# Kernel tuning notes

Measured on AMD Instinct MI355X. Metric: run time of the kernel, lower is better.

Reference implementation:

```python
import jax, jax.numpy as jnp
import numpy as np

S = 20  # number of standard amino acids; hardcoded in the original layer


def expm_fixed(A, squarings=6, terms=14):
    """Scaling-and-squaring matrix exponential with fixed squaring count.
    A: (..., n, n). tau*Q entries are small (tau ~ softplus(-3)), so a fixed
    2^-6 scaling + Taylor-14 matches tf.linalg.expm to fp32 tolerance."""
    A = A / (2.0 ** squarings)
    I = jnp.broadcast_to(jnp.eye(A.shape[-1], dtype=A.dtype), A.shape)
    out = I
    term = I
    for i in range(1, terms + 1):
        term = jnp.matmul(term, A) / i
        out = out + term
    for _ in range(squarings):
        out = jnp.matmul(out, out)
    return out


def make_rate_matrix(R, p, eps=1e-16):
    """R: (N, s, s) symmetric exchangeabilities, zero diag. p: (N, s) equilibrium."""
    Q = R * p[:, None, :]                       # Q[i,j] = R[i,j] * p[j]
    diag = jnp.sum(Q, axis=-1, keepdims=True)   # (N, s, 1)
    eye = jnp.eye(Q.shape[-1], dtype=Q.dtype)
    Q = Q - diag * eye
    mue = jnp.sum(p[:, :, None] * diag, axis=-2, keepdims=True)  # (N,1,1)
    return Q / jnp.maximum(mue, eps)


def setup_inputs() -> dict:
    key = jax.random.key(0)
    ks = jax.random.split(key, 6)
    m, b, L, k, nr = 2, 256, 1024, 4, 100
    inputs = jax.random.uniform(ks[0], (m, b, L, S), dtype=jnp.float32)
    rate_indices = jax.random.randint(ks[1], (m, b), 0, nr, dtype=jnp.int64)
    # rate_init = constant(-3.0); small jitter so gradients are non-degenerate
    tau_kernel = -3.0 + 0.1 * jax.random.normal(ks[2], (m, nr), dtype=jnp.float32)
    exchangeability_kernel = 0.1 * jax.random.normal(ks[3], (m, k, S, S), dtype=jnp.float32)
    equilibrium_kernel = 0.1 * jax.random.normal(ks[4], (m, k, S), dtype=jnp.float32)
    per_matrix_rates_kernel = 0.1 * jax.random.normal(ks[5], (m, k), dtype=jnp.float32)
    return {
        "inputs": inputs,
        "tau_kernel": tau_kernel,
        "exchangeability_kernel": exchangeability_kernel,
        "equilibrium_kernel": equilibrium_kernel,
        "per_matrix_rates_kernel": per_matrix_rates_kernel,
        "rate_indices": rate_indices,
    }


def reference(inputs, tau_kernel, exchangeability_kernel, equilibrium_kernel,
              per_matrix_rates_kernel, rate_indices):
    m, b, L, s = inputs.shape
    k = exchangeability_kernel.shape[1]
    # make_tau(subset): gather per-sequence times then softplus
    tau = jax.nn.softplus(jnp.take_along_axis(tau_kernel, rate_indices, axis=1))  # (m,b)
    # per-matrix rates
    pmr = jax.nn.softplus(per_matrix_rates_kernel)  # (m,k)
    mut_rates = tau[:, :, None] * pmr[:, None, :]   # (m,b,k)
    # make_R: symmetrize, softplus, zero diagonal
    K = exchangeability_kernel
    R = jax.nn.softplus(0.5 * (K + jnp.swapaxes(K, -1, -2)))
    R = R * (1.0 - jnp.eye(s, dtype=R.dtype))       # (m,k,s,s)
    # make_p
    p = jax.nn.softmax(equilibrium_kernel, axis=-1)  # (m,k,s)
    # normalized rate matrices
    Q = make_rate_matrix(R.reshape(-1, s, s), p.reshape(-1, s)).reshape(m, k, s, s)
    # tau * Q, batched over sequences: (m,b,k,s,s)
    tauQ = mut_rates[..., None, None] * Q[:, None]
    P = expm_fixed(tauQ.reshape(-1, s, s)).reshape(m, b, k, s, s)
    # vector-format inputs path (non-transposed): mbLz,mbkzs->mbLks
    anc = jnp.einsum('mblz,mbkzs->mblks', inputs, P)
    # documented output: (num_model, b, L, num_matrices*s)
    return anc.reshape(m, b, L, k * s)
```

## Files before the change

kernel.cpp:

```cpp
#include <hip/hip_runtime.h>
#include <math.h>

#define M_  2
#define B_  256
#define L_  1024
#define K_  4
#define S_  20
#define NR_ 100
#define NTERM 7

typedef float f32x4_t __attribute__((ext_vector_type(4)));

__device__ __forceinline__ float softplusf(float x) {
    return x > 20.0f ? x : log1pf(expf(x));
}

__global__ __launch_bounds__(512)
void qpow_kernel(const float* __restrict__ exch,
                 const float* __restrict__ equil,
                 float*       __restrict__ Qpow)
{
    __shared__ float sQ[400];
    __shared__ float sT[2][400];
    __shared__ float sRow[20];

    const int blk = blockIdx.x;
    const int kk = blk % K_;
    const int mm = blk / K_;
    const int tid = threadIdx.x;
    const bool act = tid < 400;
    const int i = tid / 20;
    const int j = tid - i * 20;

    float p[20];
    float Q0 = 0.0f, rowsum = 0.0f;

    if (act) {
        const float* eq = equil + (mm * K_ + kk) * S_;
        float mx = eq[0];
        #pragma unroll
        for (int z = 1; z < 20; ++z) mx = fmaxf(mx, eq[z]);
        float s = 0.0f;
        #pragma unroll
        for (int z = 0; z < 20; ++z) { p[z] = expf(eq[z] - mx); s += p[z]; }
        const float inv = 1.0f / s;
        #pragma unroll
        for (int z = 0; z < 20; ++z) p[z] *= inv;

        const float* Kx = exch + (mm * K_ + kk) * S_ * S_;
        float R = (i == j) ? 0.0f : softplusf(0.5f * (Kx[i * 20 + j] + Kx[j * 20 + i]));
        Q0 = R * p[j];
        sQ[tid] = Q0;
    }
    __syncthreads();

    if (act) {
        rowsum = 0.0f;
        #pragma unroll
        for (int z = 0; z < 20; ++z) rowsum += sQ[i * 20 + z];
        if (j == 0) sRow[i] = rowsum;
    }
    __syncthreads();

    float* Tout = Qpow + (size_t)blk * (NTERM * 400);
    if (act) {
        float mue = 0.0f;
        #pragma unroll
        for (int z = 0; z < 20; ++z) mue += p[z] * sRow[z];
        float q = (Q0 - ((i == j) ? rowsum : 0.0f)) / fmaxf(mue, 1e-16f);
        sQ[tid] = q;
        sT[0][tid] = q;
        Tout[tid] = q;
    }
    __syncthreads();

    int cur = 0;
    for (int n = 2; n <= NTERM; ++n) {
        if (act) {
            float acc = 0.0f;
            #pragma unroll
            for (int z = 0; z < 20; ++z) acc += sT[cur][i * 20 + z] * sQ[z * 20 + j];
            acc /= (float)n;
            sT[cur ^ 1][tid] = acc;
            Tout[(n - 1) * 400 + tid] = acc;
        }
        __syncthreads();
        cur ^= 1;
    }
}

__global__ __launch_bounds__(512)
void pbuild_kernel(const float* __restrict__ Qpow,
                   const float* __restrict__ tauk,
                   const float* __restrict__ pmrk,
                   float*       __restrict__ Pws)
{
    const int blk = blockIdx.x;
    const int kk = blk % K_;
    const int rr = (blk / K_) % NR_;
    const int mm = blk / (K_ * NR_);
    const int tid = threadIdx.x;
    if (tid >= 400) return;

    const float mu = softplusf(tauk[mm * NR_ + rr]) * softplusf(pmrk[mm * K_ + kk]);
    const float* T = Qpow + ((size_t)(mm * K_ + kk) * NTERM) * 400 + tid;

    float acc = (tid % 21 == 0) ? 1.0f : 0.0f;
    float mp = mu;
    #pragma unroll
    for (int n = 0; n < NTERM; ++n) { acc = fmaf(mp, T[n * 400], acc); mp *= mu; }
    Pws[(size_t)blk * 400 + tid] = acc;
}

#define SPANR 256
#define TPB3  320

__device__ __forceinline__ void fma4(float4& a, float s, const float4& p) {
    a.x = fmaf(s, p.x, a.x);
    a.y = fmaf(s, p.y, a.y);
    a.z = fmaf(s, p.z, a.z);
    a.w = fmaf(s, p.w, a.w);
}

__device__ __forceinline__ void nt_store4(float* dst, const float4& v) {
    f32x4_t w;
    w.x = v.x; w.y = v.y; w.z = v.z; w.w = v.w;
    __builtin_nontemporal_store(w, (f32x4_t*)dst);
}

__device__ __forceinline__ void dma16(const void* gsrc, void* lds_base) {
    __builtin_amdgcn_global_load_lds(
        (const __attribute__((address_space(1))) void*)gsrc,
        (__attribute__((address_space(3))) void*)lds_base,
        16, 0, 0);
}

__global__ __launch_bounds__(TPB3)
void einsum_kernel(const float* __restrict__ inp,
                   const float* __restrict__ Pws,
                   const int*   __restrict__ ridx,
                   float*       __restrict__ out)
{
    __shared__ float Pl[K_ * 400];
    __shared__ float inL[SPANR * 20];

    const int bx0     = blockIdx.x;
    const int bx      = (bx0 & 7) * 256 + (bx0 >> 3);
    const int quarter = bx & 3;
    const int mb      = bx >> 2;
    const int mm      = mb >> 8;
    const int tid     = threadIdx.x;
    const int wave    = tid >> 6;
    const int lane    = tid & 63;
    const int t       = tid % 20;
    const int rg      = tid / 20;
    const int k       = t / 5;
    const int s0      = (t % 5) * 4;

    const int r = ridx[mb];

    {
        const size_t row0g = (size_t)mb * L_ + (size_t)quarter * SPANR;
        const char* gin = (const char*)(inp + row0g * 20);
        char* lin = (char*)inL;
        #pragma unroll
        for (int q = 0; q < 4; ++q) {
            const int off = (q * 5 + wave) * 1024;
            dma16(gin + off + lane * 16, lin + off);
        }
        const char* gp = (const char*)(Pws + ((size_t)(mm * NR_ + r) * K_) * 400);
        char* lp = (char*)Pl;
        {
            const int off = wave * 1024;
            dma16(gp + off + lane * 16, lp + off);
        }
        if (tid < 80) {
            const int off = 5120 + wave * 1024;
            dma16(gp + off + lane * 16, lp + off);
        }
    }
    __syncthreads();

    const size_t row0 = (size_t)mb * L_ + (size_t)quarter * SPANR;
    float* ob = out + row0 * 80 + k * 20 + s0;
    const float* Pk = Pl + k * 400 + s0;

    float4 acc[16];
    #pragma unroll
    for (int rr = 0; rr < 16; ++rr) acc[rr] = make_float4(0.f, 0.f, 0.f, 0.f);

    #pragma unroll
    for (int z4 = 0; z4 < 5; ++z4) {
        const float4 p0 = *(const float4*)(Pk + (z4 * 4 + 0) * 20);
        const float4 p1 = *(const float4*)(Pk + (z4 * 4 + 1) * 20);
        const float4 p2 = *(const float4*)(Pk + (z4 * 4 + 2) * 20);
        const float4 p3 = *(const float4*)(Pk + (z4 * 4 + 3) * 20);
        #pragma unroll
        for (int rr = 0; rr < 16; ++rr) {
            const int l = rg + rr * 16;
            const float4 av = *(const float4*)(inL + l * 20 + z4 * 4);
            fma4(acc[rr], av.x, p0);
            fma4(acc[rr], av.y, p1);
            fma4(acc[rr], av.z, p2);
            fma4(acc[rr], av.w, p3);
        }
    }

    #pragma unroll
    for (int rr = 0; rr < 16; ++rr) {
        const int l = rg + rr * 16;
        nt_store4(ob + (size_t)l * 80, acc[rr]);
    }
}

extern "C" void kernel_launch(void* const* d_in, const int* in_sizes, int n_in,
                              void* d_out, int out_size, void* d_ws, size_t ws_size,
                              hipStream_t stream) {
    const float* inp   = (const float*)d_in[0];
    const float* tauk  = (const float*)d_in[1];
    const float* exch  = (const float*)d_in[2];
    const float* equil = (const float*)d_in[3];
    const float* pmrk  = (const float*)d_in[4];
    const int*   ridx  = (const int*)d_in[5];
    float* outp = (float*)d_out;

    float* Qpow = (float*)d_ws;
    float* Pws  = Qpow + (size_t)M_ * K_ * NTERM * 400;

    qpow_kernel<<<M_ * K_, 512, 0, stream>>>(exch, equil, Qpow);
    pbuild_kernel<<<M_ * NR_ * K_, 512, 0, stream>>>(Qpow, tauk, pmrk, Pws);
    einsum_kernel<<<M_ * B_ * (L_ / SPANR), TPB3, 0, stream>>>(inp, Pws, ridx, outp);
}
```

Measured before the change: 55.27 us.

## Double-buffer einsum input chunks so DMA of second chunk overlaps compute

Each einsum block now handles 512 rows as two 256-row chunks with separate LDS buffers. The second chunk's global-to-LDS DMA is issued before computing the first, then a vmcnt wait and barrier gate the second compute. This aims to hide load latency inside a block, at the cost of half as many blocks and double the LDS per block, which lowers occupancy. The vmcnt(16) count relies on the 16 nontemporal stores from the first chunk being the only memory ops issued after the second chunk's loads.

```diff
diff --git a/kernel.cpp b/kernel.cpp
--- a/kernel.cpp
+++ b/kernel.cpp
@@ -112,8 +112,8 @@
     Pws[(size_t)blk * 400 + tid] = acc;
 }
 
-#define SPANR 256
-#define TPB3  320
+#define CHUNKR 256
+#define TPB3   320
 
 __device__ __forceinline__ void fma4(float4& a, float s, const float4& p) {
     a.x = fmaf(s, p.x, a.x);
@@ -133,6 +133,45 @@
         (const __attribute__((address_space(1))) void*)gsrc,
         (__attribute__((address_space(3))) void*)lds_base,
         16, 0, 0);
+}
+
+__device__ __forceinline__ void stage_chunk(const char* gin, char* lin,
+                                            int wave, int lane) {
+    #pragma unroll
+    for (int q = 0; q < 4; ++q) {
+        const int off = (q * 5 + wave) * 1024;
+        dma16(gin + off + lane * 16, lin + off);
+    }
+}
+
+__device__ __forceinline__ void compute_chunk(const float* inbuf, const float* Pk,
+                                              float* ob, int rg) {
+    float4 acc[16];
+    #pragma unroll
+    for (int rr = 0; rr < 16; ++rr) acc[rr] = make_float4(0.f, 0.f, 0.f, 0.f);
+
+    #pragma unroll
+    for (int z4 = 0; z4 < 5; ++z4) {
+        const float4 p0 = *(const float4*)(Pk + (z4 * 4 + 0) * 20);
+        const float4 p1 = *(const float4*)(Pk + (z4 * 4 + 1) * 20);
+        const float4 p2 = *(const float4*)(Pk + (z4 * 4 + 2) * 20);
+        const float4 p3 = *(const float4*)(Pk + (z4 * 4 + 3) * 20);
+        #pragma unroll
+        for (int rr = 0; rr < 16; ++rr) {
+            const int l = rg + rr * 16;
+            const float4 av = *(const float4*)(inbuf + l * 20 + z4 * 4);
+            fma4(acc[rr], av.x, p0);
+            fma4(acc[rr], av.y, p1);
+            fma4(acc[rr], av.z, p2);
+            fma4(acc[rr], av.w, p3);
+        }
+    }
+
+    #pragma unroll
+    for (int rr = 0; rr < 16; ++rr) {
+        const int l = rg + rr * 16;
+        nt_store4(ob + (size_t)l * 80, acc[rr]);
+    }
 }
 
 __global__ __launch_bounds__(TPB3)
@@ -142,32 +181,29 @@
                    float*       __restrict__ out)
 {
     __shared__ float Pl[K_ * 400];
-    __shared__ float inL[SPANR * 20];
-
-    const int bx0     = blockIdx.x;
-    const int bx      = (bx0 & 7) * 256 + (bx0 >> 3);
-    const int quarter = bx & 3;
-    const int mb      = bx >> 2;
-    const int mm      = mb >> 8;
-    const int tid     = threadIdx.x;
-    const int wave    = tid >> 6;
-    const int lane    = tid & 63;
-    const int t       = tid % 20;
-    const int rg      = tid / 20;
-    const int k       = t / 5;
-    const int s0      = (t % 5) * 4;
+    __shared__ float inL0[CHUNKR * 20];
+    __shared__ float inL1[CHUNKR * 20];
+
+    const int bx0  = blockIdx.x;
+    const int bx   = (bx0 & 7) * 128 + (bx0 >> 3);
+    const int half = bx & 1;
+    const int mb   = bx >> 1;
+    const int mm   = mb >> 8;
+    const int tid  = threadIdx.x;
+    const int wave = tid >> 6;
+    const int lane = tid & 63;
+    const int t    = tid % 20;
+    const int rg   = tid / 20;
+    const int k    = t / 5;
+    const int s0   = (t % 5) * 4;
 
     const int r = ridx[mb];
 
+    const size_t row0 = (size_t)mb * L_ + (size_t)half * 512;
+    const char* gin = (const char*)(inp + row0 * 20);
+
+    stage_chunk(gin, (char*)inL0, wave, lane);
     {
-        const size_t row0g = (size_t)mb * L_ + (size_t)quarter * SPANR;
-        const char* gin = (const char*)(inp + row0g * 20);
-        char* lin = (char*)inL;
-        #pragma unroll
-        for (int q = 0; q < 4; ++q) {
-            const int off = (q * 5 + wave) * 1024;
-            dma16(gin + off + lane * 16, lin + off);
-        }
         const char* gp = (const char*)(Pws + ((size_t)(mm * NR_ + r) * K_) * 400);
         char* lp = (char*)Pl;
         {
@@ -181,36 +217,18 @@
     }
     __syncthreads();
 
-    const size_t row0 = (size_t)mb * L_ + (size_t)quarter * SPANR;
+    stage_chunk(gin + CHUNKR * 80, (char*)inL1, wave, lane);
+
+    const float* Pk = Pl + k * 400 + s0;
     float* ob = out + row0 * 80 + k * 20 + s0;
-    const float* Pk = Pl + k * 400 + s0;
-
-    float4 acc[16];
-    #pragma unroll
-    for (int rr = 0; rr < 16; ++rr) acc[rr] = make_float4(0.f, 0.f, 0.f, 0.f);
-
-    #pragma unroll
-    for (int z4 = 0; z4 < 5; ++z4) {
-        const float4 p0 = *(const float4*)(Pk + (z4 * 4 + 0) * 20);
-        const float4 p1 = *(const float4*)(Pk + (z4 * 4 + 1) * 20);
-        const float4 p2 = *(const float4*)(Pk + (z4 * 4 + 2) * 20);
-        const float4 p3 = *(const float4*)(Pk + (z4 * 4 + 3) * 20);
-        #pragma unroll
-        for (int rr = 0; rr < 16; ++rr) {
-            const int l = rg + rr * 16;
-            const float4 av = *(const float4*)(inL + l * 20 + z4 * 4);
-            fma4(acc[rr], av.x, p0);
-            fma4(acc[rr], av.y, p1);
-            fma4(acc[rr], av.z, p2);
-            fma4(acc[rr], av.w, p3);
-        }
-    }
-
-    #pragma unroll
-    for (int rr = 0; rr < 16; ++rr) {
-        const int l = rg + rr * 16;
-        nt_store4(ob + (size_t)l * 80, acc[rr]);
-    }
+
+    compute_chunk(inL0, Pk, ob, rg);
+
+    asm volatile("s_waitcnt vmcnt(16)" ::: "memory");
+    __builtin_amdgcn_s_barrier();
+    __builtin_amdgcn_sched_barrier(0);
+
+    compute_chunk(inL1, Pk, ob + (size_t)CHUNKR * 80, rg);
 }
 
 extern "C" void kernel_launch(void* const* d_in, const int* in_sizes, int n_in,
@@ -229,5 +247,5 @@
 
     qpow_kernel<<<M_ * K_, 512, 0, stream>>>(exch, equil, Qpow);
     pbuild_kernel<<<M_ * NR_ * K_, 512, 0, stream>>>(Qpow, tauk, pmrk, Pws);
-    einsum_kernel<<<M_ * B_ * (L_ / SPANR), TPB3, 0, stream>>>(inp, Pws, ridx, outp);
-}
+    einsum_kernel<<<M_ * B_ * (L_ / 512), TPB3, 0, stream>>>(inp, Pws, ridx, outp);
+}
```

Result: slower. 56.53 us (+2.3%).
